# Kernel optimization log

Measured on AMD Instinct MI355X. Metric: run time of the kernel, lower is better.

## Reference

```python
import jax, jax.numpy as jnp
import numpy as np

C = 32       # dim_features
D1 = 1024    # line grid resolution (dim1)
D2 = 256     # lowres plane resolution (dim2)
M = 64       # hidden width m
H = 1024
W = 1024
RESX = 1024.0
RESY = 1024.0


def setup_inputs() -> dict:
    key = jax.random.key(0)
    ks = jax.random.split(key, 8)
    coords = jax.random.uniform(ks[0], (H, W, 2), dtype=jnp.float32) * RESX
    # operation == 'multiply' init: rand*0.15 + 0.1
    line_feature_x = jax.random.uniform(ks[1], (C, D1), dtype=jnp.float32) * 0.15 + 0.1
    line_feature_y = jax.random.uniform(ks[2], (C, D1), dtype=jnp.float32) * 0.15 + 0.1
    plane_feature = jax.random.normal(ks[3], (C, D2, D2), dtype=jnp.float32) * 0.01
    W1 = jax.random.normal(ks[4], (M, C), dtype=jnp.float32) * (1.0 / np.sqrt(C))
    b1 = jnp.zeros((M,), dtype=jnp.float32)
    W2 = jax.random.normal(ks[5], (1, M), dtype=jnp.float32) * (1.0 / np.sqrt(M))
    b2 = jnp.zeros((1,), dtype=jnp.float32)
    return {"coords": coords, "line_feature_x": line_feature_x,
            "line_feature_y": line_feature_y, "plane_feature": plane_feature,
            "W1": W1, "b1": b1, "W2": W2, "b2": b2}


def _interp_line(table, gnorm):
    # table: [C, L]; gnorm: [H, W] in [-1, 1].
    # grid_sample(mode=bilinear, padding_mode=border, align_corners=True) on a
    # [1, C, L, 1] input reduces to 1D linear interp along L with clamped coords.
    L = table.shape[1]
    pos = jnp.clip((gnorm + 1.0) * 0.5 * (L - 1), 0.0, float(L - 1))
    i0 = jnp.minimum(jnp.floor(pos).astype(jnp.int32), L - 2)
    w = pos - i0.astype(pos.dtype)           # [H, W]
    return table[:, i0] * (1.0 - w) + table[:, i0 + 1] * w  # [C, H, W]


def _interp_plane(plane, xn, yn):
    # plane: [C, D, D]; xn/yn: [H, W] in [-1, 1].
    # grid_sample(mode=bilinear, padding_mode=zeros, align_corners=True).
    D = plane.shape[-1]
    px = (xn + 1.0) * 0.5 * (D - 1)
    py = (yn + 1.0) * 0.5 * (D - 1)
    x0 = jnp.floor(px).astype(jnp.int32)
    y0 = jnp.floor(py).astype(jnp.int32)
    wx = px - x0.astype(px.dtype)
    wy = py - y0.astype(py.dtype)

    def gather(yi, xi):
        valid = (xi >= 0) & (xi < D) & (yi >= 0) & (yi < D)   # zeros padding
        xc = jnp.clip(xi, 0, D - 1)
        yc = jnp.clip(yi, 0, D - 1)
        return plane[:, yc, xc] * valid                       # [C, H, W]

    return (gather(y0, x0) * (1.0 - wy) * (1.0 - wx)
            + gather(y0, x0 + 1) * (1.0 - wy) * wx
            + gather(y0 + 1, x0) * wy * (1.0 - wx)
            + gather(y0 + 1, x0 + 1) * wy * wx)


def reference(coords, line_feature_x, line_feature_y, plane_feature, W1, b1, W2, b2):
    xn = coords[..., 0] * 2.0 / RESX - 1.0   # [H, W]
    yn = coords[..., 1] * 2.0 / RESY - 1.0
    fx = _interp_line(line_feature_x, xn)    # [C, H, W]
    fy = _interp_line(line_feature_y, yn)    # [C, H, W]
    fp = _interp_plane(plane_feature, xn, yn)  # [C, H, W]
    # operation == 'multiply', mode == 'lowres'
    feat = (fx * fy + fp).transpose(1, 2, 0)  # [H, W, C]
    # nonconvex decoder: Linear(C->M) + ReLU + Linear(M->1)
    h = jax.nn.relu(jnp.einsum('hwc,mc->hwm', feat, W1) + b1)
    out = jnp.einsum('hwm,om->hwo', h, W2) + b2
    return out[..., 0]                        # [H, W]
```

## Files before the change

### kernel.cpp

```cpp
#include <hip/hip_runtime.h>

#define NC   32
#define ND1  1024
#define ND2  256
#define NM   64
#define NPIX (1024 * 1024)
#define NBUCK 256
#define CAP  4608
#define NSLOT (NBUCK * CAP)
#define PW   18
#define PPADF 36
#define FBLK 3
#define FTH  512
#define PART_SLOTS (CAP / FBLK)
#define PART_CHUNKS (PART_SLOTS/16)

typedef __attribute__((ext_vector_type(8))) short bf16x8;
typedef __attribute__((ext_vector_type(4))) float f32x4;

__device__ __forceinline__ int clampi(int v, int lo, int hi) {
    return min(max(v, lo), hi);
}

__device__ __forceinline__ void pack_hilo(const float* f, bf16x8& hi, bf16x8& lo) {
    union { unsigned int u[4]; bf16x8 v; } H, L;
#pragma unroll
    for (int j = 0; j < 4; ++j) {
        unsigned int b0 = __float_as_uint(f[2 * j]);
        unsigned int b1 = __float_as_uint(f[2 * j + 1]);
        unsigned int h0 = b0 & 0xFFFF0000u, h1 = b1 & 0xFFFF0000u;
        H.u[j] = (h0 >> 16) | h1;
        float l0 = f[2 * j]     - __uint_as_float(h0);
        float l1 = f[2 * j + 1] - __uint_as_float(h1);
        L.u[j] = (__float_as_uint(l0) >> 16) | (__float_as_uint(l1) & 0xFFFF0000u);
    }
    hi = H.v; lo = L.v;
}

__global__ __launch_bounds__(256) void pass1_prepare(
    const float* __restrict__ plane, const float* __restrict__ lfx,
    const float* __restrict__ lfy, float* __restrict__ pl_t,
    float* __restrict__ lx_t, float* __restrict__ ly_t, int* __restrict__ cursor)
{
    __shared__ float tile[32][65];
    const int blk = blockIdx.x, tid = threadIdx.x;
    const float* in; float* out; int N, pos0;
    if (blk < 16)       { in = lfx;   out = lx_t; N = 1024;  pos0 = blk * 64; }
    else if (blk < 32)  { in = lfy;   out = ly_t; N = 1024;  pos0 = (blk - 16) * 64; }
    else if (blk == 32) { if (cursor && tid < NBUCK) cursor[tid] = tid * CAP; return; }
    else                { in = plane; out = pl_t; N = 65536; pos0 = (blk - 33) * 64; }
#pragma unroll
    for (int r = 0; r < 8; ++r) {
        int c = r * 4 + (tid >> 6), p = tid & 63;
        tile[c][p] = in[c * N + pos0 + p];
    }
    __syncthreads();
#pragma unroll
    for (int r = 0; r < 8; ++r) {
        int p = r * 8 + (tid >> 5), c = tid & 31;
        out[(pos0 + p) * 32 + c] = tile[c][p];
    }
}

__global__ __launch_bounds__(1024) void scatter_slack(
    const float2* __restrict__ coords, int* __restrict__ cursor,
    float4* __restrict__ slots)
{
    __shared__ int h[NBUCK];
    __shared__ int basew[NBUCK];
    const int t = threadIdx.x;
    if (t < NBUCK) h[t] = 0;
    __syncthreads();
    const int base_i = blockIdx.x * 4096;
    float2 xy[4]; int cell[4];
#pragma unroll
    for (int r = 0; r < 4; ++r) {
        xy[r] = coords[base_i + r * 1024 + t];
        const int xi = clampi((int)xy[r].x, 0, 1023);
        const int yi = clampi((int)xy[r].y, 0, 1023);
        cell[r] = ((yi >> 6) << 4) | (xi >> 6);
        atomicAdd(&h[cell[r]], 1);
    }
    __syncthreads();
    if (t < NBUCK) {
        const int n = h[t];
        basew[t] = n ? atomicAdd(&cursor[t], n) : 0;
    }
    __syncthreads();
    if (t < NBUCK) h[t] = 0;
    __syncthreads();
#pragma unroll
    for (int r = 0; r < 4; ++r) {
        const int c   = cell[r];
        const int off = atomicAdd(&h[c], 1);
        const int dst = min(basew[c] + off, NSLOT - 1);
        slots[dst] = make_float4(xy[r].x, xy[r].y,
                                 __int_as_float(base_i + r * 1024 + t), 0.0f);
    }
}

__global__ __launch_bounds__(FTH, 4) void fused_mfma(
    const float4* __restrict__ slots, const int* __restrict__ cursor,
    const float* __restrict__ lx,
    const float* __restrict__ ly,
    const float* __restrict__ plane,
    const float* __restrict__ W1, const float* __restrict__ b1,
    const float* __restrict__ W2, const float* __restrict__ b2,
    float* __restrict__ out)
{
    const int b    = blockIdx.x / FBLK;
    const int part = blockIdx.x - b * FBLK;
    const int t    = threadIdx.x;
    const int wid  = t >> 6;
    const int lane = t & 63;
    const int lcol = lane & 15;
    const int lq   = lane >> 4;
    const int bx = b & 15, by = b >> 4;
    const int px0 = (int)(bx * 15.9375f);
    const int py0 = (int)(by * 15.9375f);

    __shared__ float pls[PW * PW * PPADF];
    for (int i = t; i < PW * PW * 32; i += FTH) {
        const int c = i / (PW * PW), tex = i - c * (PW * PW);
        const int ty = tex / PW, tx = tex - ty * PW;
        const int gy = min(py0 + ty, ND2 - 1), gx = min(px0 + tx, ND2 - 1);
        pls[tex * PPADF + c] = plane[c * 65536 + (gy << 8) + gx];
    }

    bf16x8 bhi[4], blo[4];
    float b1v[4], w2v[4];
#pragma unroll
    for (int nt = 0; nt < 4; ++nt) {
        const int row = nt * 16 + lcol;
        const float4* wr = (const float4*)(W1 + row * NC + lq * 8);
        const float4 wa = wr[0], wb = wr[1];
        float wf[8] = {wa.x, wa.y, wa.z, wa.w, wb.x, wb.y, wb.z, wb.w};
        pack_hilo(wf, bhi[nt], blo[nt]);
        b1v[nt] = b1[row];
        w2v[nt] = W2[row];
    }
    const float b2s = b2[0];
    __syncthreads();

    const int base  = b * CAP;
    const int count = min(cursor[b] - base, CAP);

    for (int ci = wid; ci < PART_CHUNKS; ci += FTH / 64) {
        const int chunk = part * PART_SLOTS + ci * 16;
        if (chunk >= count) break;
        const int s = chunk + lcol;
        const float4 rec = slots[base + min(s, count - 1)];
        const float x = rec.x, y = rec.y;

        const float xn = x * (2.0f / 1024.0f) - 1.0f;
        const float yn = y * (2.0f / 1024.0f) - 1.0f;

        float posx = fminf(fmaxf((xn + 1.0f) * 0.5f * 1023.0f, 0.0f), 1023.0f);
        int   ix   = min((int)posx, 1022);
        float wx   = posx - (float)ix, omwx = 1.0f - wx;
        float posy = fminf(fmaxf((yn + 1.0f) * 0.5f * 1023.0f, 0.0f), 1023.0f);
        int   iy   = min((int)posy, 1022);
        float wy   = posy - (float)iy, omwy = 1.0f - wy;

        float px  = (xn + 1.0f) * 0.5f * 255.0f;
        float py  = (yn + 1.0f) * 0.5f * 255.0f;
        float fx0 = floorf(px), fy0 = floorf(py);
        int   x0 = (int)fx0, y0 = (int)fy0;
        float pwx = px - fx0, pwy = py - fy0;
        int   x1 = x0 + 1, y1 = y0 + 1;
        float vx0 = (x0 >= 0 && x0 < ND2) ? 1.0f : 0.0f;
        float vx1 = (x1 >= 0 && x1 < ND2) ? 1.0f : 0.0f;
        float vy0 = (y0 >= 0 && y0 < ND2) ? 1.0f : 0.0f;
        float vy1 = (y1 >= 0 && y1 < ND2) ? 1.0f : 0.0f;
        int xc0 = clampi(x0, 0, ND2 - 1), xc1 = clampi(x1, 0, ND2 - 1);
        int yc0 = clampi(y0, 0, ND2 - 1), yc1 = clampi(y1, 0, ND2 - 1);
        float w00 = (1.0f - pwy) * (1.0f - pwx) * vy0 * vx0;
        float w01 = (1.0f - pwy) * pwx          * vy0 * vx1;
        float w10 = pwy          * (1.0f - pwx) * vy1 * vx0;
        float w11 = pwy          * pwx          * vy1 * vx1;

        const int ko = lq * 8;
        const float4* LX0 = (const float4*)(lx + ix * NC + ko);
        const float4* LX1 = (const float4*)(lx + (ix + 1) * NC + ko);
        const float4* LY0 = (const float4*)(ly + iy * NC + ko);
        const float4* LY1 = (const float4*)(ly + (iy + 1) * NC + ko);
        const float4 xa = LX0[0], xb = LX0[1], Xa = LX1[0], Xb = LX1[1];
        const float4 ya = LY0[0], yb = LY0[1], Ya = LY1[0], Yb = LY1[1];

        const int t00o = ((yc0 - py0) * PW + (xc0 - px0)) * PPADF + ko;
        const int t01o = ((yc0 - py0) * PW + (xc1 - px0)) * PPADF + ko;
        const int t10o = ((yc1 - py0) * PW + (xc0 - px0)) * PPADF + ko;
        const int t11o = ((yc1 - py0) * PW + (xc1 - px0)) * PPADF + ko;
        const float4 q00a = *(const float4*)&pls[t00o], q00b = *(const float4*)&pls[t00o + 4];
        const float4 q01a = *(const float4*)&pls[t01o], q01b = *(const float4*)&pls[t01o + 4];
        const float4 q10a = *(const float4*)&pls[t10o], q10b = *(const float4*)&pls[t10o + 4];
        const float4 q11a = *(const float4*)&pls[t11o], q11b = *(const float4*)&pls[t11o + 4];

        const float a0[8] = {xa.x, xa.y, xa.z, xa.w, xb.x, xb.y, xb.z, xb.w};
        const float a1[8] = {Xa.x, Xa.y, Xa.z, Xa.w, Xb.x, Xb.y, Xb.z, Xb.w};
        const float c0[8] = {ya.x, ya.y, ya.z, ya.w, yb.x, yb.y, yb.z, yb.w};
        const float c1[8] = {Ya.x, Ya.y, Ya.z, Ya.w, Yb.x, Yb.y, Yb.z, Yb.w};
        const float p00[8] = {q00a.x, q00a.y, q00a.z, q00a.w, q00b.x, q00b.y, q00b.z, q00b.w};
        const float p01[8] = {q01a.x, q01a.y, q01a.z, q01a.w, q01b.x, q01b.y, q01b.z, q01b.w};
        const float p10[8] = {q10a.x, q10a.y, q10a.z, q10a.w, q10b.x, q10b.y, q10b.z, q10b.w};
        const float p11[8] = {q11a.x, q11a.y, q11a.z, q11a.w, q11b.x, q11b.y, q11b.z, q11b.w};

        float f[8];
#pragma unroll
        for (int j = 0; j < 8; ++j) {
            const float fxv = a0[j] * omwx + a1[j] * wx;
            const float fyv = c0[j] * omwy + c1[j] * wy;
            const float fpv = p00[j] * w00 + p01[j] * w01 + p10[j] * w10 + p11[j] * w11;
            f[j] = fxv * fyv + fpv;
        }

        bf16x8 ahi, alo;
        pack_hilo(f, ahi, alo);

        float psum[4] = {0.0f, 0.0f, 0.0f, 0.0f};
#pragma unroll
        for (int nt = 0; nt < 4; ++nt) {
            f32x4 acc = {b1v[nt], b1v[nt], b1v[nt], b1v[nt]};
            acc = __builtin_amdgcn_mfma_f32_16x16x32_bf16(ahi, bhi[nt], acc, 0, 0, 0);
            acc = __builtin_amdgcn_mfma_f32_16x16x32_bf16(ahi, blo[nt], acc, 0, 0, 0);
            acc = __builtin_amdgcn_mfma_f32_16x16x32_bf16(alo, bhi[nt], acc, 0, 0, 0);
#pragma unroll
            for (int r = 0; r < 4; ++r)
                psum[r] = fmaf(fmaxf(acc[r], 0.0f), w2v[nt], psum[r]);
        }

#pragma unroll
        for (int m = 1; m <= 8; m <<= 1) {
#pragma unroll
            for (int r = 0; r < 4; ++r)
                psum[r] += __shfl_xor(psum[r], m, 64);
        }

        if (lq == (lcol >> 2) && s < count)
            out[__float_as_int(rec.z)] = psum[lcol & 3] + b2s;
    }
}

template <int MODE>
__global__ __launch_bounds__(256) void fused_forward(
    const float* __restrict__ coords, const float* __restrict__ lx,
    const float* __restrict__ ly, const float* __restrict__ pl,
    const float* __restrict__ W1, const float* __restrict__ b1,
    const float* __restrict__ W2, const float* __restrict__ b2,
    float* __restrict__ out)
{
    const int i = blockIdx.x * 256 + threadIdx.x;
    const float2 xy = reinterpret_cast<const float2*>(coords)[i];
    const float xn = xy.x * (2.0f / 1024.0f) - 1.0f;
    const float yn = xy.y * (2.0f / 1024.0f) - 1.0f;

    float posx = fminf(fmaxf((xn + 1.0f) * 0.5f * 1023.0f, 0.0f), 1023.0f);
    int   ix   = min((int)posx, 1022);
    float wx   = posx - (float)ix, omwx = 1.0f - wx;
    float posy = fminf(fmaxf((yn + 1.0f) * 0.5f * 1023.0f, 0.0f), 1023.0f);
    int   iy   = min((int)posy, 1022);
    float wy   = posy - (float)iy, omwy = 1.0f - wy;

    float px  = (xn + 1.0f) * 0.5f * 255.0f;
    float py  = (yn + 1.0f) * 0.5f * 255.0f;
    float fx0 = floorf(px), fy0 = floorf(py);
    int   x0 = (int)fx0, y0 = (int)fy0;
    float pwx = px - fx0, pwy = py - fy0;
    int   x1 = x0 + 1, y1 = y0 + 1;
    float vx0 = (x0 >= 0 && x0 < ND2) ? 1.0f : 0.0f;
    float vx1 = (x1 >= 0 && x1 < ND2) ? 1.0f : 0.0f;
    float vy0 = (y0 >= 0 && y0 < ND2) ? 1.0f : 0.0f;
    float vy1 = (y1 >= 0 && y1 < ND2) ? 1.0f : 0.0f;
    int xc0 = clampi(x0, 0, ND2 - 1), xc1 = clampi(x1, 0, ND2 - 1);
    int yc0 = clampi(y0, 0, ND2 - 1), yc1 = clampi(y1, 0, ND2 - 1);
    float w00 = (1.0f - pwy) * (1.0f - pwx) * vy0 * vx0;
    float w01 = (1.0f - pwy) * pwx          * vy0 * vx1;
    float w10 = pwy          * (1.0f - pwx) * vy1 * vx0;
    float w11 = pwy          * pwx          * vy1 * vx1;

    float feat[NC];
    if (MODE == 1) {
        const float4* ax0 = (const float4*)(lx + ix * NC);
        const float4* ax1 = (const float4*)(lx + (ix + 1) * NC);
        const float4* ay0 = (const float4*)(ly + iy * NC);
        const float4* ay1 = (const float4*)(ly + (iy + 1) * NC);
        const float4* p00 = (const float4*)(pl + (yc0 * ND2 + xc0) * NC);
        const float4* p01 = (const float4*)(pl + (yc0 * ND2 + xc1) * NC);
        const float4* p10 = (const float4*)(pl + (yc1 * ND2 + xc0) * NC);
        const float4* p11 = (const float4*)(pl + (yc1 * ND2 + xc1) * NC);
#pragma unroll
        for (int k = 0; k < 8; ++k) {
            float4 a0 = ax0[k], a1 = ax1[k], c0 = ay0[k], c1 = ay1[k];
            float4 q00 = p00[k], q01 = p01[k], q10 = p10[k], q11 = p11[k];
#define FC(j, comp)                                                          \
            {                                                                \
                float fxv = a0.comp * omwx + a1.comp * wx;                   \
                float fyv = c0.comp * omwy + c1.comp * wy;                   \
                float fpv = q00.comp * w00 + q01.comp * w01 +                \
                            q10.comp * w10 + q11.comp * w11;                 \
                feat[k * 4 + j] = fxv * fyv + fpv;                           \
            }
            FC(0, x) FC(1, y) FC(2, z) FC(3, w)
#undef FC
        }
    } else {
#pragma unroll
        for (int c = 0; c < NC; ++c) {
            float a0 = lx[c * ND1 + ix], a1 = lx[c * ND1 + ix + 1];
            float c0 = ly[c * ND1 + iy], c1 = ly[c * ND1 + iy + 1];
            const float* ps = pl + c * (ND2 * ND2);
            float q00 = ps[yc0 * ND2 + xc0], q01 = ps[yc0 * ND2 + xc1];
            float q10 = ps[yc1 * ND2 + xc0], q11 = ps[yc1 * ND2 + xc1];
            feat[c] = (a0 * omwx + a1 * wx) * (c0 * omwy + c1 * wy)
                    + (q00 * w00 + q01 * w01 + q10 * w10 + q11 * w11);
        }
    }

    float acc = b2[0];
#pragma unroll 4
    for (int m = 0; m < NM; ++m) {
        const float4* wrow = (const float4*)(W1 + m * NC);
        float a = b1[m];
#pragma unroll
        for (int k = 0; k < 8; ++k) {
            float4 wv = wrow[k];
            a = fmaf(feat[k * 4 + 0], wv.x, a);
            a = fmaf(feat[k * 4 + 1], wv.y, a);
            a = fmaf(feat[k * 4 + 2], wv.z, a);
            a = fmaf(feat[k * 4 + 3], wv.w, a);
        }
        acc = fmaf(fmaxf(a, 0.0f), W2[m], acc);
    }
    out[i] = acc;
}

extern "C" void kernel_launch(void* const* d_in, const int* in_sizes, int n_in,
                              void* d_out, int out_size, void* d_ws, size_t ws_size,
                              hipStream_t stream) {
    const float* coords = (const float*)d_in[0];
    const float* lfx    = (const float*)d_in[1];
    const float* lfy    = (const float*)d_in[2];
    const float* plane  = (const float*)d_in[3];
    const float* W1     = (const float*)d_in[4];
    const float* b1     = (const float*)d_in[5];
    const float* W2     = (const float*)d_in[6];
    const float* b2     = (const float*)d_in[7];
    float* out = (float*)d_out;

    const size_t planeBytes = (size_t)ND2 * ND2 * NC * sizeof(float);
    const size_t lineBytes  = (size_t)ND1 * NC * sizeof(float);
    const size_t slotsBytes = (size_t)NSLOT * sizeof(float4);
    const size_t needTrans  = planeBytes + 2 * lineBytes;
    const size_t needFull   = needTrans + slotsBytes + NBUCK * sizeof(int);

    if (ws_size >= needFull) {
        char* p = (char*)d_ws;
        float*  pl_t   = (float*)p;   p += planeBytes;
        float*  lx_t   = (float*)p;   p += lineBytes;
        float*  ly_t   = (float*)p;   p += lineBytes;
        float4* slots  = (float4*)p;  p += slotsBytes;
        int*    cursor = (int*)p;

        pass1_prepare<<<33, 256, 0, stream>>>(plane, lfx, lfy,
                                              pl_t, lx_t, ly_t, cursor);
        scatter_slack<<<NPIX / 4096, 1024, 0, stream>>>((const float2*)coords,
                                                        cursor, slots);
        fused_mfma<<<NBUCK * FBLK, FTH, 0, stream>>>(slots, cursor, lx_t, ly_t,
                                                     plane, W1, b1, W2, b2, out);
    } else if (ws_size >= needTrans) {
        float* pl_t = (float*)d_ws;
        float* lx_t = (float*)((char*)d_ws + planeBytes);
        float* ly_t = lx_t + ND1 * NC;
        pass1_prepare<<<1057, 256, 0, stream>>>(plane, lfx, lfy,
                                                pl_t, lx_t, ly_t, nullptr);
        fused_forward<1><<<NPIX / 256, 256, 0, stream>>>(
            coords, lx_t, ly_t, pl_t, W1, b1, W2, b2, out);
    } else {
        fused_forward<0><<<NPIX / 256, 256, 0, stream>>>(
            coords, lfx, lfy, plane, W1, b1, W2, b2, out);
    }
}
```

Measured before the change: 195.1 us.

## Store plane tile in LDS as bf16 from transposed layout, split buckets four ways

The fused kernel now loads its plane tile from the channel-last transposed plane, which pass1_prepare now fully produces (1057 blocks instead of 33), using float4 reads. It stores the tile in LDS as bf16, halving LDS footprint and read traffic, and unpacks to float during interpolation. FBLK goes from 3 to 4 for more blocks per bucket, and the scatter kernel reuses the first atomic's offsets instead of a second histogram pass. The bf16 rounding of plane features adds approximation error, and the larger prepare pass adds a full plane transpose.

Measured after the change: 177.6 us. 9.0% less time.

```diff
diff --git a/kernel.cpp b/kernel.cpp
--- a/kernel.cpp
+++ b/kernel.cpp
@@ -9,8 +9,8 @@
 #define CAP  4608
 #define NSLOT (NBUCK * CAP)
 #define PW   18
-#define PPADF 36
-#define FBLK 3
+#define PWS  40
+#define FBLK 4
 #define FTH  512
 #define PART_SLOTS (CAP / FBLK)
 #define PART_CHUNKS (PART_SLOTS/16)
@@ -20,6 +20,10 @@
 
 __device__ __forceinline__ int clampi(int v, int lo, int hi) {
     return min(max(v, lo), hi);
+}
+
+__device__ __forceinline__ unsigned int bf16rne(float f) {
+    return (__float_as_uint(f) + 0x8000u) >> 16;
 }
 
 __device__ __forceinline__ void pack_hilo(const float* f, bf16x8& hi, bf16x8& lo) {
@@ -72,14 +76,14 @@
     if (t < NBUCK) h[t] = 0;
     __syncthreads();
     const int base_i = blockIdx.x * 4096;
-    float2 xy[4]; int cell[4];
+    float2 xy[4]; int cell[4]; int off[4];
 #pragma unroll
     for (int r = 0; r < 4; ++r) {
         xy[r] = coords[base_i + r * 1024 + t];
         const int xi = clampi((int)xy[r].x, 0, 1023);
         const int yi = clampi((int)xy[r].y, 0, 1023);
         cell[r] = ((yi >> 6) << 4) | (xi >> 6);
-        atomicAdd(&h[cell[r]], 1);
+        off[r] = atomicAdd(&h[cell[r]], 1);
     }
     __syncthreads();
     if (t < NBUCK) {
@@ -87,13 +91,9 @@
         basew[t] = n ? atomicAdd(&cursor[t], n) : 0;
     }
     __syncthreads();
-    if (t < NBUCK) h[t] = 0;
-    __syncthreads();
 #pragma unroll
     for (int r = 0; r < 4; ++r) {
-        const int c   = cell[r];
-        const int off = atomicAdd(&h[c], 1);
-        const int dst = min(basew[c] + off, NSLOT - 1);
+        const int dst = min(basew[cell[r]] + off[r], NSLOT - 1);
         slots[dst] = make_float4(xy[r].x, xy[r].y,
                                  __int_as_float(base_i + r * 1024 + t), 0.0f);
     }
@@ -103,7 +103,7 @@
     const float4* __restrict__ slots, const int* __restrict__ cursor,
     const float* __restrict__ lx,
     const float* __restrict__ ly,
-    const float* __restrict__ plane,
+    const float* __restrict__ pl,
     const float* __restrict__ W1, const float* __restrict__ b1,
     const float* __restrict__ W2, const float* __restrict__ b2,
     float* __restrict__ out)
@@ -119,12 +119,16 @@
     const int px0 = (int)(bx * 15.9375f);
     const int py0 = (int)(by * 15.9375f);
 
-    __shared__ float pls[PW * PW * PPADF];
-    for (int i = t; i < PW * PW * 32; i += FTH) {
-        const int c = i / (PW * PW), tex = i - c * (PW * PW);
+    __shared__ __align__(16) unsigned short pls[PW * PW * PWS];
+    for (int i = t; i < PW * PW * 8; i += FTH) {
+        const int tex = i >> 3, k4 = i & 7;
         const int ty = tex / PW, tx = tex - ty * PW;
         const int gy = min(py0 + ty, ND2 - 1), gx = min(px0 + tx, ND2 - 1);
-        pls[tex * PPADF + c] = plane[c * 65536 + (gy << 8) + gx];
+        const float4 v = ((const float4*)pl)[((gy << 8) + gx) * 8 + k4];
+        uint2 pk;
+        pk.x = bf16rne(v.x) | (bf16rne(v.y) << 16);
+        pk.y = bf16rne(v.z) | (bf16rne(v.w) << 16);
+        *(uint2*)&pls[tex * PWS + k4 * 4] = pk;
     }
 
     bf16x8 bhi[4], blo[4];
@@ -187,31 +191,45 @@
         const float4 xa = LX0[0], xb = LX0[1], Xa = LX1[0], Xb = LX1[1];
         const float4 ya = LY0[0], yb = LY0[1], Ya = LY1[0], Yb = LY1[1];
 
-        const int t00o = ((yc0 - py0) * PW + (xc0 - px0)) * PPADF + ko;
-        const int t01o = ((yc0 - py0) * PW + (xc1 - px0)) * PPADF + ko;
-        const int t10o = ((yc1 - py0) * PW + (xc0 - px0)) * PPADF + ko;
-        const int t11o = ((yc1 - py0) * PW + (xc1 - px0)) * PPADF + ko;
-        const float4 q00a = *(const float4*)&pls[t00o], q00b = *(const float4*)&pls[t00o + 4];
-        const float4 q01a = *(const float4*)&pls[t01o], q01b = *(const float4*)&pls[t01o + 4];
-        const float4 q10a = *(const float4*)&pls[t10o], q10b = *(const float4*)&pls[t10o + 4];
-        const float4 q11a = *(const float4*)&pls[t11o], q11b = *(const float4*)&pls[t11o + 4];
+        const uint4 u00 = *(const uint4*)&pls[((yc0 - py0) * PW + (xc0 - px0)) * PWS + ko];
+        const uint4 u01 = *(const uint4*)&pls[((yc0 - py0) * PW + (xc1 - px0)) * PWS + ko];
+        const uint4 u10 = *(const uint4*)&pls[((yc1 - py0) * PW + (xc0 - px0)) * PWS + ko];
+        const uint4 u11 = *(const uint4*)&pls[((yc1 - py0) * PW + (xc1 - px0)) * PWS + ko];
 
         const float a0[8] = {xa.x, xa.y, xa.z, xa.w, xb.x, xb.y, xb.z, xb.w};
         const float a1[8] = {Xa.x, Xa.y, Xa.z, Xa.w, Xb.x, Xb.y, Xb.z, Xb.w};
         const float c0[8] = {ya.x, ya.y, ya.z, ya.w, yb.x, yb.y, yb.z, yb.w};
         const float c1[8] = {Ya.x, Ya.y, Ya.z, Ya.w, Yb.x, Yb.y, Yb.z, Yb.w};
-        const float p00[8] = {q00a.x, q00a.y, q00a.z, q00a.w, q00b.x, q00b.y, q00b.z, q00b.w};
-        const float p01[8] = {q01a.x, q01a.y, q01a.z, q01a.w, q01b.x, q01b.y, q01b.z, q01b.w};
-        const float p10[8] = {q10a.x, q10a.y, q10a.z, q10a.w, q10b.x, q10b.y, q10b.z, q10b.w};
-        const float p11[8] = {q11a.x, q11a.y, q11a.z, q11a.w, q11b.x, q11b.y, q11b.z, q11b.w};
+
+        const unsigned int uu00[4] = {u00.x, u00.y, u00.z, u00.w};
+        const unsigned int uu01[4] = {u01.x, u01.y, u01.z, u01.w};
+        const unsigned int uu10[4] = {u10.x, u10.y, u10.z, u10.w};
+        const unsigned int uu11[4] = {u11.x, u11.y, u11.z, u11.w};
 
         float f[8];
 #pragma unroll
-        for (int j = 0; j < 8; ++j) {
-            const float fxv = a0[j] * omwx + a1[j] * wx;
-            const float fyv = c0[j] * omwy + c1[j] * wy;
-            const float fpv = p00[j] * w00 + p01[j] * w01 + p10[j] * w10 + p11[j] * w11;
-            f[j] = fxv * fyv + fpv;
+        for (int j2 = 0; j2 < 4; ++j2) {
+            const float p00a = __uint_as_float(uu00[j2] << 16);
+            const float p00b = __uint_as_float(uu00[j2] & 0xFFFF0000u);
+            const float p01a = __uint_as_float(uu01[j2] << 16);
+            const float p01b = __uint_as_float(uu01[j2] & 0xFFFF0000u);
+            const float p10a = __uint_as_float(uu10[j2] << 16);
+            const float p10b = __uint_as_float(uu10[j2] & 0xFFFF0000u);
+            const float p11a = __uint_as_float(uu11[j2] << 16);
+            const float p11b = __uint_as_float(uu11[j2] & 0xFFFF0000u);
+            const int j = j2 * 2;
+            {
+                const float fxv = a0[j] * omwx + a1[j] * wx;
+                const float fyv = c0[j] * omwy + c1[j] * wy;
+                const float fpv = p00a * w00 + p01a * w01 + p10a * w10 + p11a * w11;
+                f[j] = fxv * fyv + fpv;
+            }
+            {
+                const float fxv = a0[j + 1] * omwx + a1[j + 1] * wx;
+                const float fyv = c0[j + 1] * omwy + c1[j + 1] * wy;
+                const float fpv = p00b * w00 + p01b * w01 + p10b * w10 + p11b * w11;
+                f[j + 1] = fxv * fyv + fpv;
+            }
         }
 
         bf16x8 ahi, alo;
@@ -361,12 +379,12 @@
         float4* slots  = (float4*)p;  p += slotsBytes;
         int*    cursor = (int*)p;
 
-        pass1_prepare<<<33, 256, 0, stream>>>(plane, lfx, lfy,
-                                              pl_t, lx_t, ly_t, cursor);
+        pass1_prepare<<<1057, 256, 0, stream>>>(plane, lfx, lfy,
+                                                pl_t, lx_t, ly_t, cursor);
         scatter_slack<<<NPIX / 4096, 1024, 0, stream>>>((const float2*)coords,
                                                         cursor, slots);
         fused_mfma<<<NBUCK * FBLK, FTH, 0, stream>>>(slots, cursor, lx_t, ly_t,
-                                                     plane, W1, b1, W2, b2, out);
+                                                     pl_t, W1, b1, W2, b2, out);
     } else if (ws_size >= needTrans) {
         float* pl_t = (float*)d_ws;
         float* lx_t = (float*)((char*)d_ws + planeBytes);
```
